# Kernel tuning notes

Hardware: AMD Instinct MI355X
Metric: run time of the kernel (lower is better)

## Reference

```python
import jax, jax.numpy as jnp
import numpy as np

B, T, D = 8, 1024, 512
V = 8192  # codebook_size


def setup_inputs() -> dict:
    key = jax.random.key(0)
    k1, k2, k3 = jax.random.split(key, 3)
    scale_w = float(np.sqrt(2.0 / (D + V)))  # xavier_uniform-ish scale
    scale_c = float(np.sqrt(2.0 / (V + D)))
    return {
        "inputs": jax.random.normal(k1, (B, T, D), dtype=jnp.float32),
        "codebook": jax.random.normal(k2, (V, D), dtype=jnp.float32) * scale_c,
        "W_logits": jax.random.normal(k3, (V, D), dtype=jnp.float32) * scale_w,
        "b_logits": jnp.zeros((V,), dtype=jnp.float32),
    }


def reference(inputs, codebook, W_logits, b_logits):
    # logits = Linear(input_dim -> codebook_size)
    logits = jnp.einsum("btd,vd->btv", inputs, W_logits) + b_logits  # [B,T,V]
    # eval mode: no gumbel noise, no temperature division
    soft_tokens = jax.nn.softmax(logits, axis=-1)
    token_indices = jnp.argmax(soft_tokens, axis=-1)  # [B,T]
    hard_tokens = jax.nn.one_hot(token_indices, codebook.shape[0], dtype=soft_tokens.dtype)
    # straight-through: hard values, soft gradients
    tokens_for_lookup = soft_tokens + jax.lax.stop_gradient(hard_tokens - soft_tokens)
    quantized = jnp.einsum("btv,vd->btd", tokens_for_lookup, codebook)  # [B,T,D]
    commitment_loss = jnp.mean((quantized - jax.lax.stop_gradient(inputs)) ** 2)
    return quantized, token_indices, commitment_loss, soft_tokens, logits
```

## Files before the change

kernel.cpp:

```cpp
#include <hip/hip_runtime.h>
#include <hip/hip_bf16.h>

#define BT_ 8192
#define D_  512
#define V_  8192

#define OFF_Q      0
#define OFF_TOK    4194304
#define OFF_LOSS   4202496
#define OFF_SOFT   4202497
#define OFF_LOGITS 71311361
#define STAGE_F    62922752

#define TAU  0.02f
#define EXP_NEG_TAU 0.98019867f
#define MAXC 64

typedef __attribute__((ext_vector_type(8))) short bf16x8;
typedef __attribute__((ext_vector_type(4))) float f32x4;
typedef __attribute__((ext_vector_type(4))) unsigned short u16x4;

__device__ __forceinline__ unsigned short bf16rne(float f) {
  unsigned int u = __float_as_uint(f);
  return (unsigned short)((u + 0x7fffu + ((u >> 16) & 1u)) >> 16);
}

__global__ __launch_bounds__(256) void to_bf16_k(const f32x4* __restrict__ x,
                                                 const f32x4* __restrict__ w,
                                                 u16x4* __restrict__ xa,
                                                 u16x4* __restrict__ wb) {
  const int n4 = (BT_ * D_) / 4;
  const int half = gridDim.x >> 1;
  const bool isw = blockIdx.x >= half;
  const f32x4* __restrict__ s = isw ? w : x;
  u16x4* __restrict__ d = isw ? wb : xa;
  const int b0 = isw ? blockIdx.x - half : blockIdx.x;
  for (int i = b0 * 256 + threadIdx.x; i < n4; i += half * 256) {
    const f32x4 v = s[i];
    u16x4 o;
    o[0] = bf16rne(v[0]); o[1] = bf16rne(v[1]);
    o[2] = bf16rne(v[2]); o[3] = bf16rne(v[3]);
    d[i] = o;
  }
}

__device__ __forceinline__ void gload_lds16(const void* g, void* l) {
  __builtin_amdgcn_global_load_lds((const __attribute__((address_space(1))) void*)g,
                                   (__attribute__((address_space(3))) void*)l,
                                   16, 0, 0);
}

__device__ __forceinline__ void barf() {
  __builtin_amdgcn_s_barrier();
  asm volatile("" ::: "memory");
}
__device__ __forceinline__ void vmcnt2() { asm volatile("s_waitcnt vmcnt(2)" ::: "memory"); }
__device__ __forceinline__ void vmcnt0() { asm volatile("s_waitcnt vmcnt(0)" ::: "memory"); }

__device__ __forceinline__ void stage_unit(const char* __restrict__ tb, char* ldsRegion,
                                           int ktile, int half, int wid, int lane) {
#pragma unroll
  for (int issue = 0; issue < 2; ++issue) {
    const int d = half * 16384 + issue * 8192 + wid * 1024 + lane * 16;
    const int l = d ^ (((d >> 7) & 7) << 4);
    gload_lds16(tb + (size_t)(l >> 7) * 1024 + ktile * 128 + (l & 127),
                ldsRegion + half * 16384 + issue * 8192 + wid * 1024);
  }
}

__device__ __forceinline__ bf16x8 rdfrag(const char* base, int R, int ks, int g) {
  return *(const bf16x8*)(base + R * 128 + ((ks * 64 + 16 * g) ^ ((R & 7) << 4)));
}

__device__ __forceinline__ void kgroup(int t, int smode, char* lds,
                                       const char* __restrict__ Ab,
                                       const char* __restrict__ Bb,
                                       int wr, int wc, int lane, int wid,
                                       f32x4 (&acc)[8][4]) {
  char* aL = lds + (t & 1) * 32768;
  char* bL = lds + 65536 + (t & 1) * 32768;
  char* aS = lds + ((t & 1) ^ 1) * 32768;
  char* bS = lds + 65536 + ((t & 1) ^ 1) * 32768;
  const int cg = lane & 15, g = lane >> 4;
  bf16x8 a[4][2], b0[2][2], b1[2][2];

#pragma unroll
  for (int m = 0; m < 4; ++m)
#pragma unroll
    for (int ks = 0; ks < 2; ++ks)
      a[m][ks] = rdfrag(aL, wr * 128 + m * 16 + cg, ks, g);
#pragma unroll
  for (int n = 0; n < 2; ++n)
#pragma unroll
    for (int ks = 0; ks < 2; ++ks)
      b0[n][ks] = rdfrag(bL, wc * 64 + n * 16 + cg, ks, g);
  if (smode >= 1) stage_unit(Ab, aS, t + 1, 1, wid, lane);
  barf();
  __builtin_amdgcn_s_setprio(1);
#pragma unroll
  for (int m = 0; m < 4; ++m)
#pragma unroll
    for (int n = 0; n < 2; ++n)
#pragma unroll
      for (int ks = 0; ks < 2; ++ks)
        acc[m][n] = __builtin_amdgcn_mfma_f32_16x16x32_bf16(a[m][ks], b0[n][ks], acc[m][n], 0, 0, 0);
  __builtin_amdgcn_s_setprio(0);
  barf();

#pragma unroll
  for (int n = 0; n < 2; ++n)
#pragma unroll
    for (int ks = 0; ks < 2; ++ks)
      b1[n][ks] = rdfrag(bL, wc * 64 + (n + 2) * 16 + cg, ks, g);
  if (smode >= 1) stage_unit(Bb, bS, t + 1, 0, wid, lane);
  barf();
  __builtin_amdgcn_s_setprio(1);
#pragma unroll
  for (int m = 0; m < 4; ++m)
#pragma unroll
    for (int n = 0; n < 2; ++n)
#pragma unroll
      for (int ks = 0; ks < 2; ++ks)
        acc[m][n + 2] = __builtin_amdgcn_mfma_f32_16x16x32_bf16(a[m][ks], b1[n][ks], acc[m][n + 2], 0, 0, 0);
  __builtin_amdgcn_s_setprio(0);
  barf();

#pragma unroll
  for (int m = 0; m < 4; ++m)
#pragma unroll
    for (int ks = 0; ks < 2; ++ks)
      a[m][ks] = rdfrag(aL, wr * 128 + (m + 4) * 16 + cg, ks, g);
  if (smode >= 1) stage_unit(Bb, bS, t + 1, 1, wid, lane);
  barf();
  __builtin_amdgcn_s_setprio(1);
#pragma unroll
  for (int m = 0; m < 4; ++m)
#pragma unroll
    for (int n = 0; n < 2; ++n)
#pragma unroll
      for (int ks = 0; ks < 2; ++ks)
        acc[m + 4][n + 2] = __builtin_amdgcn_mfma_f32_16x16x32_bf16(a[m][ks], b1[n][ks], acc[m + 4][n + 2], 0, 0, 0);
  __builtin_amdgcn_s_setprio(0);
  barf();

  if (smode == 2) stage_unit(Ab, aL, t + 2, 0, wid, lane);
  barf();
  __builtin_amdgcn_s_setprio(1);
#pragma unroll
  for (int m = 0; m < 4; ++m)
#pragma unroll
    for (int n = 0; n < 2; ++n)
#pragma unroll
      for (int ks = 0; ks < 2; ++ks)
        acc[m + 4][n] = __builtin_amdgcn_mfma_f32_16x16x32_bf16(a[m][ks], b0[n][ks], acc[m + 4][n], 0, 0, 0);
  __builtin_amdgcn_s_setprio(0);
  if (smode == 2) vmcnt2();
  else if (smode == 1) vmcnt0();
  barf();
}

__global__ __launch_bounds__(512) void gemm8(const unsigned short* __restrict__ A,
                                             const unsigned short* __restrict__ B,
                                             const float* __restrict__ bias,
                                             float* __restrict__ C) {
  __shared__ char lds[131072];
  const int tid  = threadIdx.x;
  const int lane = tid & 63;
  const int wid  = tid >> 6;
  const int wr   = wid >> 2, wc = wid & 3;

  const int bid = blockIdx.x;
  const int xcd = bid & 7;
  const int s   = bid >> 3;
  const int by  = (xcd >> 1) * 8 + (s >> 4);
  const int bx  = (xcd & 1) * 16 + (s & 15);
  const int row0 = by * 256, col0 = bx * 256;

  const char* Ab = (const char*)A + (size_t)row0 * (D_ * 2);
  const char* Bb = (const char*)B + (size_t)col0 * (D_ * 2);

  f32x4 acc[8][4] = {};

  stage_unit(Ab, lds, 0, 0, wid, lane);
  stage_unit(Ab, lds, 0, 1, wid, lane);
  stage_unit(Bb, lds + 65536, 0, 0, wid, lane);
  stage_unit(Bb, lds + 65536, 0, 1, wid, lane);
  stage_unit(Ab, lds + 32768, 1, 0, wid, lane);
  vmcnt2();
  barf();

  for (int t = 0; t < 6; ++t)
    kgroup(t, 2, lds, Ab, Bb, wr, wc, lane, wid, acc);
  kgroup(6, 1, lds, Ab, Bb, wr, wc, lane, wid, acc);
  kgroup(7, 0, lds, Ab, Bb, wr, wc, lane, wid, acc);

  const int cg = lane & 15, g = lane >> 4;
  float bv[4];
#pragma unroll
  for (int n = 0; n < 4; ++n) bv[n] = bias[col0 + wc * 64 + n * 16 + cg];

  float* cl = (float*)lds;
  __syncthreads();
#pragma unroll
  for (int h = 0; h < 2; ++h) {
    if (wr == h) {
#pragma unroll
      for (int m = 0; m < 8; ++m)
#pragma unroll
        for (int n = 0; n < 4; ++n) {
          const int cw = ((wc * 64 + n * 16 + cg) + 253) & 255;
#pragma unroll
          for (int rr = 0; rr < 4; ++rr) {
            const int R = m * 16 + 4 * g + rr;
            cl[R * 256 + cw] = acc[m][n][rr] + bv[n];
          }
        }
    }
    __syncthreads();
#pragma unroll
    for (int k = 0; k < 16; ++k) {
      const int r = wid * 16 + k;
      const f32x4 v = *(const f32x4*)((char*)cl + r * 1024 + lane * 16);
      const int grow = row0 + h * 128 + r;
      float* Crow = C + (size_t)grow * V_ + col0;
      if (lane < 63) {
        *((f32x4*)(Crow + 3) + lane) = v;
      } else {
        Crow[255] = v[0]; Crow[0] = v[1]; Crow[1] = v[2]; Crow[2] = v[3];
      }
    }
    __syncthreads();
  }
}

__global__ __launch_bounds__(256) void row_finish(const float* __restrict__ logits,
                                                  const float* __restrict__ xf,
                                                  const float* __restrict__ wf,
                                                  const float* __restrict__ bias,
                                                  float* __restrict__ tokf,
                                                  float* __restrict__ soft) {
  const int b    = blockIdx.x;
  const int gen  = 3 - (b >> 11);
  const int idx  = b & 2047;
  const int p    = idx >> 8;
  const int by   = (p >> 1) * 8 + gen * 2 + (p & 1);
  const int row  = by * 256 + (idx & 255);
  const int tid  = threadIdx.x;
  const int lane = tid & 63;
  const int wv   = tid >> 6;

  __shared__ float redM[4], redS[4];
  __shared__ int   cnum;
  __shared__ int   cidx[MAXC];

  const float* L = logits + (size_t)row * V_;
  float*       S = soft   + (size_t)row * V_;
  const f32x4* L4 = (const f32x4*)(L + 3);
  f32x4*       S4 = (f32x4*)(S + 3);

  f32x4 e[8];
  float m_e = 0.f, s = 0.f;
#pragma unroll
  for (int j = 0; j < 8; ++j) {
    const int i = j * 256 + tid;
    if (i < 2047) {
      const f32x4 v = L4[i];
      f32x4 t;
      t[0] = __expf(v[0]); t[1] = __expf(v[1]);
      t[2] = __expf(v[2]); t[3] = __expf(v[3]);
      e[j] = t;
      m_e = fmaxf(m_e, fmaxf(fmaxf(t[0], t[1]), fmaxf(t[2], t[3])));
      s += t[0] + t[1] + t[2] + t[3];
    } else {
      e[j][0] = 0.f; e[j][1] = 0.f; e[j][2] = 0.f; e[j][3] = 0.f;
    }
  }
  float extra_e = 0.f;
  int   extra_col = -1;
  if (tid < 3)       extra_col = tid;
  else if (tid == 3) extra_col = 8191;
  if (extra_col >= 0) {
    extra_e = __expf(L[extra_col]);
    m_e = fmaxf(m_e, extra_e);
    s += extra_e;
  }
#pragma unroll
  for (int o = 1; o < 64; o <<= 1) {
    m_e = fmaxf(m_e, __shfl_xor(m_e, o));
    s += __shfl_xor(s, o);
  }
  if (lane == 0) { redM[wv] = m_e; redS[wv] = s; }
  if (tid == 0) cnum = 0;
  __syncthreads();
  m_e = fmaxf(fmaxf(redM[0], redM[1]), fmaxf(redM[2], redM[3]));
  s   = redS[0] + redS[1] + redS[2] + redS[3];
  const float si    = 1.0f / s;
  const float thr_e = m_e * EXP_NEG_TAU;

#pragma unroll
  for (int j = 0; j < 8; ++j) {
    const int i = j * 256 + tid;
#pragma unroll
    for (int q = 0; q < 4; ++q)
      if (e[j][q] >= thr_e) {
        const int pp = atomicAdd(&cnum, 1);
        if (pp < MAXC) cidx[pp] = 3 + 4 * i + q;
      }
  }
  if (extra_col >= 0 && extra_e >= thr_e) {
    const int pp = atomicAdd(&cnum, 1);
    if (pp < MAXC) cidx[pp] = extra_col;
  }
  __syncthreads();

  if (wv == 0) {
    const int cnt = min(cnum, MAXC);
    float bestv = -1e30f;
    int   besti = 0x7fffffff;
    const float4* xr4 = (const float4*)(xf + (size_t)row * D_);
    for (int c = 0; c < cnt; ++c) {
      const int col = cidx[c];
      const float4* wr4 = (const float4*)(wf + (size_t)col * D_);
      float pr = 0.f;
#pragma unroll
      for (int q = 0; q < 2; ++q) {
        const float4 av = xr4[lane + 64 * q];
        const float4 bvv = wr4[lane + 64 * q];
        pr += av.x * bvv.x + av.y * bvv.y + av.z * bvv.z + av.w * bvv.w;
      }
#pragma unroll
      for (int o = 1; o < 64; o <<= 1) pr += __shfl_xor(pr, o);
      const float tot = pr + bias[col];
      if (tot > bestv || (tot == bestv && col < besti)) { bestv = tot; besti = col; }
    }
    if (lane == 0) tokf[row] = (float)besti;
  }

#pragma unroll
  for (int j = 0; j < 8; ++j) {
    const int i = j * 256 + tid;
    if (i < 2047) {
      f32x4 o;
      o[0] = e[j][0] * si; o[1] = e[j][1] * si;
      o[2] = e[j][2] * si; o[3] = e[j][3] * si;
      __builtin_nontemporal_store(o, S4 + i);
    }
  }
  if (extra_col >= 0) S[extra_col] = extra_e * si;
}

__global__ __launch_bounds__(256) void finalize_k(const float* __restrict__ tokf,
                                                  const float* __restrict__ cb,
                                                  const float* __restrict__ xf,
                                                  float* __restrict__ q,
                                                  float* __restrict__ loss) {
  const int row  = blockIdx.x * 4 + (threadIdx.x >> 6);
  const int lane = threadIdx.x & 63;
  const int idx  = (int)tokf[row];
  const f32x4* cr = (const f32x4*)(cb + (size_t)idx * D_);
  const f32x4* xr = (const f32x4*)(xf + (size_t)row * D_);
  f32x4* qr = (f32x4*)(q + (size_t)row * D_);
  float ls = 0.f;
#pragma unroll
  for (int j = 0; j < 2; ++j) {
    const int c = lane + j * 64;
    const f32x4 cv = cr[c];
    const f32x4 xv = xr[c];
    __builtin_nontemporal_store(cv, qr + c);
    const float dx = cv[0] - xv[0], dy = cv[1] - xv[1], dz = cv[2] - xv[2], dw = cv[3] - xv[3];
    ls += dx * dx + dy * dy + dz * dz + dw * dw;
  }
#pragma unroll
  for (int o = 32; o; o >>= 1) ls += __shfl_xor(ls, o);
  if (lane == 0) atomicAdd(loss, ls * (1.0f / 4194304.0f));
}

extern "C" void kernel_launch(void* const* d_in, const int* in_sizes, int n_in,
                              void* d_out, int out_size, void* d_ws, size_t ws_size,
                              hipStream_t stream) {
  const float* x  = (const float*)d_in[0];
  const float* cb = (const float*)d_in[1];
  const float* wl = (const float*)d_in[2];
  const float* bl = (const float*)d_in[3];
  float* out = (float*)d_out;

  float* qout   = out + OFF_Q;
  float* tokf   = out + OFF_TOK;
  float* loss   = out + OFF_LOSS;
  float* soft   = out + OFF_SOFT;
  float* logits = out + OFF_LOGITS;

  unsigned short* Abf = (unsigned short*)(out + STAGE_F);
  unsigned short* Wbf = Abf + (size_t)BT_ * D_;

  hipMemsetAsync(loss, 0, 4, stream);

  to_bf16_k<<<2048, 256, 0, stream>>>((const f32x4*)x, (const f32x4*)wl,
                                      (u16x4*)Abf, (u16x4*)Wbf);
  gemm8<<<1024, 512, 0, stream>>>(Abf, Wbf, bl, logits);
  row_finish<<<8192, 256, 0, stream>>>(logits, x, wl, bl, tokf, soft);
  finalize_k<<<2048, 256, 0, stream>>>(tokf, cb, x, qout, loss);
}
```

Measured before the change: 324.0 us.

## Restructure GEMM k-loop into two phases and fold loss memset into convert kernel

```diff
diff --git a/kernel.cpp b/kernel.cpp
--- a/kernel.cpp
+++ b/kernel.cpp
@@ -28,7 +28,9 @@
 __global__ __launch_bounds__(256) void to_bf16_k(const f32x4* __restrict__ x,
                                                  const f32x4* __restrict__ w,
                                                  u16x4* __restrict__ xa,
-                                                 u16x4* __restrict__ wb) {
+                                                 u16x4* __restrict__ wb,
+                                                 float* __restrict__ loss) {
+  if (blockIdx.x == 0 && threadIdx.x == 0) *loss = 0.f;
   const int n4 = (BT_ * D_) / 4;
   const int half = gridDim.x >> 1;
   const bool isw = blockIdx.x >= half;
@@ -54,8 +56,9 @@
   __builtin_amdgcn_s_barrier();
   asm volatile("" ::: "memory");
 }
+__device__ __forceinline__ void vmcnt0() { asm volatile("s_waitcnt vmcnt(0)" ::: "memory"); }
 __device__ __forceinline__ void vmcnt2() { asm volatile("s_waitcnt vmcnt(2)" ::: "memory"); }
-__device__ __forceinline__ void vmcnt0() { asm volatile("s_waitcnt vmcnt(0)" ::: "memory"); }
+__device__ __forceinline__ void vmcnt4() { asm volatile("s_waitcnt vmcnt(4)" ::: "memory"); }
 
 __device__ __forceinline__ void stage_unit(const char* __restrict__ tb, char* ldsRegion,
                                            int ktile, int half, int wid, int lane) {
@@ -65,6 +68,18 @@
     const int l = d ^ (((d >> 7) & 7) << 4);
     gload_lds16(tb + (size_t)(l >> 7) * 1024 + ktile * 128 + (l & 127),
                 ldsRegion + half * 16384 + issue * 8192 + wid * 1024);
+  }
+}
+
+__device__ __forceinline__ void stage_unitA(const char* __restrict__ tb, char* ldsRegion,
+                                            int ktile, int u, int wid, int lane) {
+#pragma unroll
+  for (int issue = 0; issue < 2; ++issue) {
+    const int rowbase = issue * 128 + u * 64;
+    const int dd = rowbase * 128 + wid * 1024 + lane * 16;
+    const int l = dd ^ (((dd >> 7) & 7) << 4);
+    gload_lds16(tb + (size_t)(l >> 7) * 1024 + ktile * 128 + (l & 127),
+                ldsRegion + rowbase * 128 + wid * 1024);
   }
 }
 
@@ -82,7 +97,7 @@
   char* aS = lds + ((t & 1) ^ 1) * 32768;
   char* bS = lds + 65536 + ((t & 1) ^ 1) * 32768;
   const int cg = lane & 15, g = lane >> 4;
-  bf16x8 a[4][2], b0[2][2], b1[2][2];
+  bf16x8 a[4][2], b[4][2];
 
 #pragma unroll
   for (int m = 0; m < 4; ++m)
@@ -90,39 +105,25 @@
     for (int ks = 0; ks < 2; ++ks)
       a[m][ks] = rdfrag(aL, wr * 128 + m * 16 + cg, ks, g);
 #pragma unroll
-  for (int n = 0; n < 2; ++n)
+  for (int n = 0; n < 4; ++n)
 #pragma unroll
     for (int ks = 0; ks < 2; ++ks)
-      b0[n][ks] = rdfrag(bL, wc * 64 + n * 16 + cg, ks, g);
-  if (smode >= 1) stage_unit(Ab, aS, t + 1, 1, wid, lane);
+      b[n][ks] = rdfrag(bL, wc * 64 + n * 16 + cg, ks, g);
+  if (smode >= 1) {
+    stage_unit(Bb, bS, t + 1, 0, wid, lane);
+    stage_unit(Bb, bS, t + 1, 1, wid, lane);
+  }
   barf();
   __builtin_amdgcn_s_setprio(1);
 #pragma unroll
   for (int m = 0; m < 4; ++m)
 #pragma unroll
-    for (int n = 0; n < 2; ++n)
+    for (int n = 0; n < 4; ++n)
 #pragma unroll
       for (int ks = 0; ks < 2; ++ks)
-        acc[m][n] = __builtin_amdgcn_mfma_f32_16x16x32_bf16(a[m][ks], b0[n][ks], acc[m][n], 0, 0, 0);
+        acc[m][n] = __builtin_amdgcn_mfma_f32_16x16x32_bf16(a[m][ks], b[n][ks], acc[m][n], 0, 0, 0);
   __builtin_amdgcn_s_setprio(0);
-  barf();
-
-#pragma unroll
-  for (int n = 0; n < 2; ++n)
-#pragma unroll
-    for (int ks = 0; ks < 2; ++ks)
-      b1[n][ks] = rdfrag(bL, wc * 64 + (n + 2) * 16 + cg, ks, g);
-  if (smode >= 1) stage_unit(Bb, bS, t + 1, 0, wid, lane);
-  barf();
-  __builtin_amdgcn_s_setprio(1);
-#pragma unroll
-  for (int m = 0; m < 4; ++m)
-#pragma unroll
-    for (int n = 0; n < 2; ++n)
-#pragma unroll
-      for (int ks = 0; ks < 2; ++ks)
-        acc[m][n + 2] = __builtin_amdgcn_mfma_f32_16x16x32_bf16(a[m][ks], b1[n][ks], acc[m][n + 2], 0, 0, 0);
-  __builtin_amdgcn_s_setprio(0);
+  if (smode >= 1) vmcnt4(); else vmcnt0();
   barf();
 
 #pragma unroll
@@ -130,32 +131,21 @@
 #pragma unroll
     for (int ks = 0; ks < 2; ++ks)
       a[m][ks] = rdfrag(aL, wr * 128 + (m + 4) * 16 + cg, ks, g);
-  if (smode >= 1) stage_unit(Bb, bS, t + 1, 1, wid, lane);
+  if (smode >= 1) {
+    stage_unitA(Ab, aS, t + 1, 0, wid, lane);
+    stage_unitA(Ab, aS, t + 1, 1, wid, lane);
+  }
   barf();
   __builtin_amdgcn_s_setprio(1);
 #pragma unroll
   for (int m = 0; m < 4; ++m)
 #pragma unroll
-    for (int n = 0; n < 2; ++n)
+    for (int n = 0; n < 4; ++n)
 #pragma unroll
       for (int ks = 0; ks < 2; ++ks)
-        acc[m + 4][n + 2] = __builtin_amdgcn_mfma_f32_16x16x32_bf16(a[m][ks], b1[n][ks], acc[m + 4][n + 2], 0, 0, 0);
+        acc[m + 4][n] = __builtin_amdgcn_mfma_f32_16x16x32_bf16(a[m][ks], b[n][ks], acc[m + 4][n], 0, 0, 0);
   __builtin_amdgcn_s_setprio(0);
-  barf();
-
-  if (smode == 2) stage_unit(Ab, aL, t + 2, 0, wid, lane);
-  barf();
-  __builtin_amdgcn_s_setprio(1);
-#pragma unroll
-  for (int m = 0; m < 4; ++m)
-#pragma unroll
-    for (int n = 0; n < 2; ++n)
-#pragma unroll
-      for (int ks = 0; ks < 2; ++ks)
-        acc[m + 4][n] = __builtin_amdgcn_mfma_f32_16x16x32_bf16(a[m][ks], b0[n][ks], acc[m + 4][n], 0, 0, 0);
-  __builtin_amdgcn_s_setprio(0);
-  if (smode == 2) vmcnt2();
-  else if (smode == 1) vmcnt0();
+  if (smode >= 1) vmcnt2();
   barf();
 }
 
@@ -181,17 +171,15 @@
 
   f32x4 acc[8][4] = {};
 
-  stage_unit(Ab, lds, 0, 0, wid, lane);
-  stage_unit(Ab, lds, 0, 1, wid, lane);
   stage_unit(Bb, lds + 65536, 0, 0, wid, lane);
   stage_unit(Bb, lds + 65536, 0, 1, wid, lane);
-  stage_unit(Ab, lds + 32768, 1, 0, wid, lane);
+  stage_unitA(Ab, lds, 0, 0, wid, lane);
+  stage_unitA(Ab, lds, 0, 1, wid, lane);
   vmcnt2();
   barf();
 
-  for (int t = 0; t < 6; ++t)
-    kgroup(t, 2, lds, Ab, Bb, wr, wc, lane, wid, acc);
-  kgroup(6, 1, lds, Ab, Bb, wr, wc, lane, wid, acc);
+  for (int t = 0; t < 7; ++t)
+    kgroup(t, 1, lds, Ab, Bb, wr, wc, lane, wid, acc);
   kgroup(7, 0, lds, Ab, Bb, wr, wc, lane, wid, acc);
 
   const int cg = lane & 15, g = lane >> 4;
@@ -393,10 +381,8 @@
   unsigned short* Abf = (unsigned short*)(out + STAGE_F);
   unsigned short* Wbf = Abf + (size_t)BT_ * D_;
 
-  hipMemsetAsync(loss, 0, 4, stream);
-
   to_bf16_k<<<2048, 256, 0, stream>>>((const f32x4*)x, (const f32x4*)wl,
-                                      (u16x4*)Abf, (u16x4*)Wbf);
+                                      (u16x4*)Abf, (u16x4*)Wbf, loss);
   gemm8<<<1024, 512, 0, stream>>>(Abf, Wbf, bl, logits);
   row_finish<<<8192, 256, 0, stream>>>(logits, x, wl, bl, tokf, soft);
   finalize_k<<<2048, 256, 0, stream>>>(tokf, cb, x, qout, loss);
```

After: 321.8 us. About the same (-0.7%).
